# Performance work log

Hardware: AMD Instinct MI355X
Metric: run time of the kernel (lower is better)

Reference implementation:

```python
import jax, jax.numpy as jnp
import numpy as np
import math

H = 16          # num_head
HID = 1024      # hidden_size
D = HID // H    # per-head dim used in 1/sqrt(D) scaling


def _linear(x, w, b):
    # torch nn.Linear: y = x @ W^T + b, W: [out, in]
    return jnp.einsum('bld,od->blo', x, w) + b


def _split_heads(x):
    # [B, L, HID] -> [B*H, L, D] with index b*H + h (matches transpose_qkv)
    B, L, _ = x.shape
    return x.reshape(B, L, H, D).transpose(0, 2, 1, 3).reshape(B * H, L, D)


def _merge_heads(x, B):
    # [B*H, L, D] -> [B, L, HID] (matches restore_qkv)
    BH, L, d = x.shape
    return x.reshape(B, H, L, d).transpose(0, 2, 1, 3).reshape(B, L, H * d)


def setup_inputs() -> dict:
    key = jax.random.key(0)
    ks = jax.random.split(key, 16)
    B, L = 4, 1024
    inv = 1.0 / math.sqrt(HID)
    inp = {
        'queries': jax.random.normal(ks[0], (B, L, HID), jnp.float32),
        'keys':    jax.random.normal(ks[1], (B, L, HID), jnp.float32),
        'values':  jax.random.normal(ks[2], (B, L, HID), jnp.float32),
        'prev':    jax.random.normal(ks[3], (B * H, L, L), jnp.float32),
        'mask':    jax.random.randint(ks[4], (B, L), 1, L + 1, jnp.int64),
        'Wq_w': jax.random.uniform(ks[5], (HID, HID), jnp.float32, -inv, inv),
        'Wq_b': jax.random.uniform(ks[6], (HID,), jnp.float32, -inv, inv),
        'Wk_w': jax.random.uniform(ks[7], (HID, HID), jnp.float32, -inv, inv),
        'Wk_b': jax.random.uniform(ks[8], (HID,), jnp.float32, -inv, inv),
        'Wv_w': jax.random.uniform(ks[9], (HID, HID), jnp.float32, -inv, inv),
        'Wv_b': jax.random.uniform(ks[10], (HID,), jnp.float32, -inv, inv),
        'Wo_w': jax.random.uniform(ks[11], (HID, HID), jnp.float32, -inv, inv),
        'Wo_b': jax.random.uniform(ks[12], (HID,), jnp.float32, -inv, inv),
        'gat':  jnp.asarray(1.0, jnp.float32),
    }
    return inp


def reference(queries, keys, values, prev, mask,
              Wq_w, Wq_b, Wk_w, Wk_b, Wv_w, Wv_b, Wo_w, Wo_b, gat):
    B, L, _ = queries.shape
    q = _split_heads(_linear(queries, Wq_w, Wq_b))   # [BH, L, D]
    k = _split_heads(_linear(keys,    Wk_w, Wk_b))
    v = _split_heads(_linear(values,  Wv_w, Wv_b))

    scores = jnp.einsum('bqd,bkd->bqk', q, k)        # [BH, L, L]

    # residual score gate (learn_gat=True): scalar sigmoid blend
    g = jax.nn.sigmoid(gat)
    scores = prev * g + (1.0 - g) * scores

    # masking: torch repeats mask along dim0 (tile), arange(key_len) < lengths
    lens = jnp.tile(mask, (H, 1))                    # [BH, L]
    keep = jnp.arange(L)[None, None, :] < lens[:, :, None]  # [BH, L, L]
    masked = jnp.where(keep, scores, jnp.float32(-1e9)) / math.sqrt(D)
    probs = jax.nn.softmax(masked, axis=-1)          # dropout p=0 -> identity

    att = jnp.einsum('bqk,bkd->bqd', probs, v)       # [BH, L, D]
    out = _linear(_merge_heads(att, B), Wo_w, Wo_b)  # [B, L, HID]
    return out, scores
```

## Files before the change

kernel.cpp:

```cpp
#include <hip/hip_runtime.h>
#include <hip/hip_bf16.h>
#include <stdint.h>

#define AS1 __attribute__((address_space(1)))
#define AS3 __attribute__((address_space(3)))

typedef __bf16 bf16_t;
typedef bf16_t bf16x8 __attribute__((ext_vector_type(8)));
typedef float f32x4 __attribute__((ext_vector_type(4)));
typedef unsigned short u16;
typedef u16 u16x4 __attribute__((ext_vector_type(4)));

#define MFMA16(a, b, c) __builtin_amdgcn_mfma_f32_16x16x32_bf16(a, b, c, 0, 0, 0)

static __device__ __forceinline__ void gload_lds16(const void* g, void* l) {
    __builtin_amdgcn_global_load_lds((const AS1 void*)g, (AS3 void*)l, 16, 0, 0);
}

template <int ROW_SHIFT>
static __device__ __forceinline__ void stage16k(const char* g, char* lds, int gstride, int tid) {
    const int lane = tid & 63, w = tid >> 6;
#pragma unroll
    for (int i = 0; i < 4; ++i) {
        int chunk = w + i * 4;
        int p = chunk * 1024 + lane * 16;
        int row = p >> ROW_SHIFT;
        int col = (p & ((1 << ROW_SHIFT) - 1)) ^ ((row & 7) << 4);
        gload_lds16(g + row * gstride + col, lds + chunk * 1024);
    }
}

template <int ROW_SHIFT>
static __device__ __forceinline__ bf16x8 lds_frag(const char* lds, int row, int colb) {
    int off = (row << ROW_SHIFT) + (colb ^ ((row & 7) << 4));
    return *(const bf16x8*)(lds + off);
}

__global__ __launch_bounds__(256) void pack_bf16(
    const float* q, const float* k, const float* v,
    const float* wq, const float* wk, const float* wv, const float* wo,
    bf16_t* qb, bf16_t* kb, bf16_t* vb,
    bf16_t* wqb, bf16_t* wkb, bf16_t* wvb, bf16_t* wob) {
    const float* src; bf16_t* dst; int n;
    switch (blockIdx.y) {
        case 0: src = q;  dst = qb;  n = 4194304; break;
        case 1: src = k;  dst = kb;  n = 4194304; break;
        case 2: src = v;  dst = vb;  n = 4194304; break;
        case 3: src = wq; dst = wqb; n = 1048576; break;
        case 4: src = wk; dst = wkb; n = 1048576; break;
        case 5: src = wv; dst = wvb; n = 1048576; break;
        default: src = wo; dst = wob; n = 1048576; break;
    }
    int i = (blockIdx.x * 256 + threadIdx.x) * 8;
    if (i >= n) return;
    f32x4 v0 = *(const f32x4*)(src + i);
    f32x4 v1 = *(const f32x4*)(src + i + 4);
    bf16x8 o;
#pragma unroll
    for (int e = 0; e < 4; ++e) o[e] = (bf16_t)v0[e];
#pragma unroll
    for (int e = 0; e < 4; ++e) o[e + 4] = (bf16_t)v1[e];
    *(bf16x8*)(dst + i) = o;
}

template <int MODE>
__global__ __launch_bounds__(256, 2) void gemm_nt(
    const bf16_t* A0, const bf16_t* A1, const bf16_t* A2,
    const bf16_t* B0, const bf16_t* B1, const bf16_t* B2,
    const float* bias0, const float* bias1, const float* bias2,
    bf16_t* Qs, bf16_t* Ks, bf16_t* Vt, float* outF) {
    __shared__ __align__(1024) char sm[32768];
    const int tid = threadIdx.x, lane = tid & 63, w = tid >> 6;
    const int wr = w >> 1, wc = w & 1;
    const int m0 = blockIdx.y * 128, n0 = blockIdx.x * 128;
    const int z = (MODE == 0) ? blockIdx.z : 0;

    const bf16_t* A; const bf16_t* Bw; const float* bias;
    if (MODE == 0) {
        A    = (z == 0) ? A0 : (z == 1) ? A1 : A2;
        Bw   = (z == 0) ? B0 : (z == 1) ? B1 : B2;
        bias = (z == 0) ? bias0 : (z == 1) ? bias1 : bias2;
    } else { A = A0; Bw = B0; bias = bias0; }

    const char* Ab = (const char*)A + (size_t)m0 * 2048;
    const char* Bb = (const char*)Bw + (size_t)n0 * 2048;

    f32x4 acc[4][4] = {};
    for (int k0 = 0; k0 < 1024; k0 += 64) {
        stage16k<7>(Ab + k0 * 2, sm, 2048, tid);
        stage16k<7>(Bb + k0 * 2, sm + 16384, 2048, tid);
        __syncthreads();
#pragma unroll
        for (int kk = 0; kk < 2; ++kk) {
            bf16x8 af[4], bfr[4];
#pragma unroll
            for (int i = 0; i < 4; ++i)
                af[i] = lds_frag<7>(sm, wr * 64 + i * 16 + (lane & 15), kk * 64 + (lane >> 4) * 16);
#pragma unroll
            for (int j = 0; j < 4; ++j)
                bfr[j] = lds_frag<7>(sm + 16384, wc * 64 + j * 16 + (lane & 15), kk * 64 + (lane >> 4) * 16);
#pragma unroll
            for (int i = 0; i < 4; ++i)
#pragma unroll
                for (int j = 0; j < 4; ++j)
                    acc[i][j] = MFMA16(af[i], bfr[j], acc[i][j]);
        }
        __syncthreads();
    }

#pragma unroll
    for (int i = 0; i < 4; ++i) {
#pragma unroll
        for (int j = 0; j < 4; ++j) {
            const int mb = m0 + wr * 64 + i * 16 + ((lane >> 4) << 2);
            const int n = n0 + wc * 64 + j * 16 + (lane & 15);
            const float bv = bias[n];
            if (MODE == 1) {
#pragma unroll
                for (int r = 0; r < 4; ++r)
                    outF[(size_t)(mb + r) * 1024 + n] = acc[i][j][r] + bv;
            } else if (z == 2) {
                const int b = mb >> 10, l = mb & 1023;
                const int h = n >> 6, d = n & 63;
                u16x4 pk;
#pragma unroll
                for (int r = 0; r < 4; ++r) {
                    bf16_t x = (bf16_t)(acc[i][j][r] + bv);
                    pk[r] = __builtin_bit_cast(u16, x);
                }
                *(u16x4*)&Vt[((size_t)((b * 16 + h) * 64 + d)) * 1024 + l] = pk;
            } else {
                bf16_t* dst = (z == 0) ? Qs : Ks;
                const int h = n >> 6, d = n & 63;
#pragma unroll
                for (int r = 0; r < 4; ++r) {
                    const int m = mb + r, b = m >> 10, l = m & 1023;
                    dst[((size_t)((b * 16 + h) * 1024 + l)) * 64 + d] = (bf16_t)(acc[i][j][r] + bv);
                }
            }
        }
    }
}

__global__ __launch_bounds__(256) void attn_scores(
    const bf16_t* Qs, const bf16_t* Ks,
    const float* prev, const int* mask, const float* gatp,
    float* scoresOut, float* rowMax, float* rowSum) {
    const int tid = threadIdx.x, lane = tid & 63, w = tid >> 6;
    const int bh = blockIdx.y;
    const int q0 = blockIdx.x * 64 + w * 16;
    const float gv = gatp[0];
    const float g = 1.f / (1.f + __expf(-gv));
    const float og = 1.f - g;

    bf16x8 qa[2];
#pragma unroll
    for (int kk = 0; kk < 2; ++kk)
        qa[kk] = *(const bf16x8*)(Qs + ((size_t)(bh * 1024 + q0 + (lane & 15))) * 64 + kk * 32 + (lane >> 4) * 8);

    const int rq = q0 + ((lane >> 4) << 2);
    int len[4]; float mrun[4], lrun[4];
#pragma unroll
    for (int r = 0; r < 4; ++r) {
        len[r] = mask[(bh & 3) * 1024 + rq + r];
        mrun[r] = -1e30f;
        lrun[r] = 0.f;
    }

    const bf16_t* Kb = Ks + (size_t)bh * 65536;
    const float* prow = prev + ((size_t)(bh * 1024 + rq)) * 1024;
    float* srow = scoresOut + ((size_t)(bh * 1024 + rq)) * 1024;

    for (int kt = 0; kt < 8; ++kt) {
        const int kcb = kt * 128 + (lane & 15);
        float pf[8][4];
#pragma unroll
        for (int j = 0; j < 8; ++j)
#pragma unroll
            for (int r = 0; r < 4; ++r)
                pf[j][r] = prow[(size_t)r * 1024 + kcb + j * 16];

        f32x4 s[8] = {};
#pragma unroll
        for (int kk = 0; kk < 2; ++kk)
#pragma unroll
            for (int j = 0; j < 8; ++j) {
                bf16x8 bfr = *(const bf16x8*)(Kb + ((size_t)(kt * 128 + j * 16 + (lane & 15))) * 64 + kk * 32 + (lane >> 4) * 8);
                s[j] = MFMA16(qa[kk], bfr, s[j]);
            }

#pragma unroll
        for (int j = 0; j < 8; ++j)
#pragma unroll
            for (int r = 0; r < 4; ++r) {
                const float bl = g * pf[j][r] + og * s[j][r];
                srow[(size_t)r * 1024 + kcb + j * 16] = bl;
                s[j][r] = bl * 0.125f;
            }

#pragma unroll
        for (int r = 0; r < 4; ++r) {
            const int ln = len[r];
            float vm = -1e30f;
#pragma unroll
            for (int j = 0; j < 8; ++j)
                vm = fmaxf(vm, (kcb + j * 16 < ln) ? s[j][r] : -1e30f);
            vm = fmaxf(vm, __shfl_xor(vm, 1));
            vm = fmaxf(vm, __shfl_xor(vm, 2));
            vm = fmaxf(vm, __shfl_xor(vm, 4));
            vm = fmaxf(vm, __shfl_xor(vm, 8));
            const float mnew = fmaxf(mrun[r], vm);
            float es = 0.f;
#pragma unroll
            for (int j = 0; j < 8; ++j)
                es += (kcb + j * 16 < ln) ? __expf(s[j][r] - mnew) : 0.f;
            es += __shfl_xor(es, 1);
            es += __shfl_xor(es, 2);
            es += __shfl_xor(es, 4);
            es += __shfl_xor(es, 8);
            lrun[r] = lrun[r] * __expf(mrun[r] - mnew) + es;
            mrun[r] = mnew;
        }
    }
    if ((lane & 15) == 0) {
#pragma unroll
        for (int r = 0; r < 4; ++r) {
            rowMax[bh * 1024 + rq + r] = mrun[r];
            rowSum[bh * 1024 + rq + r] = lrun[r];
        }
    }
}

__global__ __launch_bounds__(256) void attn_pv(
    const float* scoresOut, const bf16_t* Vt,
    const int* mask, const float* rowMax, const float* rowSum,
    bf16_t* att) {
    const int tid = threadIdx.x, lane = tid & 63, w = tid >> 6;
    const int bh = blockIdx.y;
    const int q0 = blockIdx.x * 64 + w * 16;
    const int qrow = q0 + (lane & 15);
    const float mq = rowMax[bh * 1024 + qrow];
    const float il = 1.f / rowSum[bh * 1024 + qrow];
    const int len = mask[(bh & 3) * 1024 + qrow];

    const float* srow = scoresOut + ((size_t)(bh * 1024 + qrow)) * 1024;
    const bf16_t* Vb = Vt + (size_t)bh * 65536;

    f32x4 acc[4] = {};
    for (int kt = 0; kt < 8; ++kt) {
        const int kb0 = kt * 128 + (lane >> 4) * 8;
        f32x4 sv[4][2];
#pragma unroll
        for (int kk = 0; kk < 4; ++kk) {
            sv[kk][0] = *(const f32x4*)(srow + kb0 + kk * 32);
            sv[kk][1] = *(const f32x4*)(srow + kb0 + kk * 32 + 4);
        }
#pragma unroll
        for (int kk = 0; kk < 4; ++kk) {
            bf16x8 pa;
#pragma unroll
            for (int e = 0; e < 8; ++e) {
                const float vv = (e < 4) ? sv[kk][0][e] : sv[kk][1][e - 4];
                pa[e] = (bf16_t)((kb0 + kk * 32 + e < len) ? __expf(vv * 0.125f - mq) * il : 0.f);
            }
#pragma unroll
            for (int ni = 0; ni < 4; ++ni) {
                bf16x8 vb = *(const bf16x8*)(Vb + ((size_t)(ni * 16 + (lane & 15))) * 1024 + kt * 128 + kk * 32 + (lane >> 4) * 8);
                acc[ni] = MFMA16(pa, vb, acc[ni]);
            }
        }
    }
    const int b = bh >> 4, h = bh & 15;
    const int rq = q0 + ((lane >> 4) << 2);
#pragma unroll
    for (int ni = 0; ni < 4; ++ni) {
        const int d = ni * 16 + (lane & 15);
#pragma unroll
        for (int r = 0; r < 4; ++r)
            att[((size_t)(b * 1024 + rq + r)) * 1024 + h * 64 + d] = (bf16_t)acc[ni][r];
    }
}

extern "C" void kernel_launch(void* const* d_in, const int* in_sizes, int n_in,
                              void* d_out, int out_size, void* d_ws, size_t ws_size,
                              hipStream_t stream) {
    (void)in_sizes; (void)n_in; (void)out_size; (void)ws_size;
    const float* q    = (const float*)d_in[0];
    const float* k    = (const float*)d_in[1];
    const float* v    = (const float*)d_in[2];
    const float* prev = (const float*)d_in[3];
    const int*   mask = (const int*)d_in[4];
    const float* Wq_w = (const float*)d_in[5];
    const float* Wq_b = (const float*)d_in[6];
    const float* Wk_w = (const float*)d_in[7];
    const float* Wk_b = (const float*)d_in[8];
    const float* Wv_w = (const float*)d_in[9];
    const float* Wv_b = (const float*)d_in[10];
    const float* Wo_w = (const float*)d_in[11];
    const float* Wo_b = (const float*)d_in[12];
    const float* gat  = (const float*)d_in[13];

    float* outp   = (float*)d_out;
    float* scores = outp + 4194304;

    char* ws = (char*)d_ws;
    bf16_t* qb  = (bf16_t*)(ws + 0);
    bf16_t* kb  = (bf16_t*)(ws + 8388608);
    bf16_t* vb  = (bf16_t*)(ws + 16777216);
    bf16_t* wqb = (bf16_t*)(ws + 25165824);
    bf16_t* wkb = (bf16_t*)(ws + 27262976);
    bf16_t* wvb = (bf16_t*)(ws + 29360128);
    bf16_t* wob = (bf16_t*)(ws + 31457280);
    bf16_t* Qs  = (bf16_t*)(ws + 33554432);
    bf16_t* Ks  = (bf16_t*)(ws + 41943040);
    bf16_t* Vt  = (bf16_t*)(ws + 50331648);
    bf16_t* att = (bf16_t*)(ws + 58720256);
    float* rowMax = (float*)(ws + 67108864);
    float* rowSum = (float*)(ws + 67371008);

    pack_bf16<<<dim3(2048, 7), 256, 0, stream>>>(q, k, v, Wq_w, Wk_w, Wv_w, Wo_w,
                                                 qb, kb, vb, wqb, wkb, wvb, wob);
    gemm_nt<0><<<dim3(8, 32, 3), 256, 0, stream>>>(qb, kb, vb, wqb, wkb, wvb,
                                                   Wq_b, Wk_b, Wv_b, Qs, Ks, Vt, nullptr);
    attn_scores<<<dim3(16, 64), 256, 0, stream>>>(Qs, Ks, prev, mask, gat,
                                                  scores, rowMax, rowSum);
    attn_pv<<<dim3(16, 64), 256, 0, stream>>>(scores, Vt, mask, rowMax, rowSum, att);
    gemm_nt<1><<<dim3(8, 32, 1), 256, 0, stream>>>(att, nullptr, nullptr, wob, nullptr, nullptr,
                                                   Wo_b, nullptr, nullptr,
                                                   nullptr, nullptr, nullptr, outp);
}
```

Measured before the change: 745.0 us.

## Fuse score and PV kernels into single flash-style online-softmax attention kernel

After: 682.8 us. -8.3%, faster.

```diff
diff --git a/kernel.cpp b/kernel.cpp
--- a/kernel.cpp
+++ b/kernel.cpp
@@ -7,6 +7,7 @@
 
 typedef __bf16 bf16_t;
 typedef bf16_t bf16x8 __attribute__((ext_vector_type(8)));
+typedef bf16_t bf16x4 __attribute__((ext_vector_type(4)));
 typedef float f32x4 __attribute__((ext_vector_type(4)));
 typedef unsigned short u16;
 typedef u16 u16x4 __attribute__((ext_vector_type(4)));
@@ -142,143 +143,129 @@
     }
 }
 
-__global__ __launch_bounds__(256) void attn_scores(
-    const bf16_t* Qs, const bf16_t* Ks,
+__global__ __launch_bounds__(256) void attn_fused(
+    const bf16_t* Qs, const bf16_t* Ks, const bf16_t* Vt,
     const float* prev, const int* mask, const float* gatp,
-    float* scoresOut, float* rowMax, float* rowSum) {
+    float* scoresOut, bf16_t* att) {
+    __shared__ __align__(1024) char psm[16384];
     const int tid = threadIdx.x, lane = tid & 63, w = tid >> 6;
+    char* myP = psm + w * 4096;
     const int bh = blockIdx.y;
     const int q0 = blockIdx.x * 64 + w * 16;
-    const float gv = gatp[0];
-    const float g = 1.f / (1.f + __expf(-gv));
-    const float og = 1.f - g;
+    const int qc = lane & 15;
+    const int gq = lane >> 4;
+    const float gate = 1.f / (1.f + __expf(-gatp[0]));
+    const float og = 1.f - gate;
 
     bf16x8 qa[2];
 #pragma unroll
     for (int kk = 0; kk < 2; ++kk)
-        qa[kk] = *(const bf16x8*)(Qs + ((size_t)(bh * 1024 + q0 + (lane & 15))) * 64 + kk * 32 + (lane >> 4) * 8);
-
-    const int rq = q0 + ((lane >> 4) << 2);
-    int len[4]; float mrun[4], lrun[4];
-#pragma unroll
-    for (int r = 0; r < 4; ++r) {
-        len[r] = mask[(bh & 3) * 1024 + rq + r];
-        mrun[r] = -1e30f;
-        lrun[r] = 0.f;
-    }
+        qa[kk] = *(const bf16x8*)(Qs + ((size_t)(bh * 1024 + q0 + qc)) * 64 + kk * 32 + gq * 8);
+
+    const int len = mask[(bh & 3) * 1024 + q0 + qc];
+    float mrun = -1e30f, lrun = 0.f;
+    f32x4 acc[4] = {};
 
     const bf16_t* Kb = Ks + (size_t)bh * 65536;
-    const float* prow = prev + ((size_t)(bh * 1024 + rq)) * 1024;
-    float* srow = scoresOut + ((size_t)(bh * 1024 + rq)) * 1024;
+    const bf16_t* Vb = Vt + (size_t)bh * 65536;
+    const float* prow = prev + ((size_t)(bh * 1024 + q0 + qc)) * 1024;
+    float* srow = scoresOut + ((size_t)(bh * 1024 + q0 + qc)) * 1024;
 
     for (int kt = 0; kt < 8; ++kt) {
-        const int kcb = kt * 128 + (lane & 15);
-        float pf[8][4];
+        const int kb = kt * 128;
+        f32x4 pf[8];
 #pragma unroll
         for (int j = 0; j < 8; ++j)
+            pf[j] = *(const f32x4*)(prow + kb + j * 16 + gq * 4);
+
+        f32x4 s[8] = {};
+#pragma unroll
+        for (int kk = 0; kk < 2; ++kk)
+#pragma unroll
+            for (int j = 0; j < 8; ++j) {
+                bf16x8 ka = *(const bf16x8*)(Kb + ((size_t)(kb + j * 16 + qc)) * 64 + kk * 32 + gq * 8);
+                s[j] = MFMA16(ka, qa[kk], s[j]);
+            }
+
+#pragma unroll
+        for (int j = 0; j < 8; ++j) {
+            f32x4 bl;
+#pragma unroll
+            for (int r = 0; r < 4; ++r) bl[r] = gate * pf[j][r] + og * s[j][r];
+            *(f32x4*)(srow + kb + j * 16 + gq * 4) = bl;
 #pragma unroll
             for (int r = 0; r < 4; ++r)
-                pf[j][r] = prow[(size_t)r * 1024 + kcb + j * 16];
-
-        f32x4 s[8] = {};
-#pragma unroll
-        for (int kk = 0; kk < 2; ++kk)
-#pragma unroll
-            for (int j = 0; j < 8; ++j) {
-                bf16x8 bfr = *(const bf16x8*)(Kb + ((size_t)(kt * 128 + j * 16 + (lane & 15))) * 64 + kk * 32 + (lane >> 4) * 8);
-                s[j] = MFMA16(qa[kk], bfr, s[j]);
+                s[j][r] = (kb + j * 16 + gq * 4 + r < len) ? bl[r] * 0.125f : -1e30f;
+        }
+
+        float vm = -1e30f;
+#pragma unroll
+        for (int j = 0; j < 8; ++j)
+#pragma unroll
+            for (int r = 0; r < 4; ++r) vm = fmaxf(vm, s[j][r]);
+        vm = fmaxf(vm, __shfl_xor(vm, 16));
+        vm = fmaxf(vm, __shfl_xor(vm, 32));
+        const float mnew = fmaxf(mrun, vm);
+
+        float ps = 0.f;
+#pragma unroll
+        for (int j = 0; j < 8; ++j)
+#pragma unroll
+            for (int r = 0; r < 4; ++r) {
+                const float p = __expf(s[j][r] - mnew);
+                s[j][r] = p;
+                ps += p;
             }
-
-#pragma unroll
-        for (int j = 0; j < 8; ++j)
-#pragma unroll
-            for (int r = 0; r < 4; ++r) {
-                const float bl = g * pf[j][r] + og * s[j][r];
-                srow[(size_t)r * 1024 + kcb + j * 16] = bl;
-                s[j][r] = bl * 0.125f;
-            }
-
-#pragma unroll
-        for (int r = 0; r < 4; ++r) {
-            const int ln = len[r];
-            float vm = -1e30f;
-#pragma unroll
-            for (int j = 0; j < 8; ++j)
-                vm = fmaxf(vm, (kcb + j * 16 < ln) ? s[j][r] : -1e30f);
-            vm = fmaxf(vm, __shfl_xor(vm, 1));
-            vm = fmaxf(vm, __shfl_xor(vm, 2));
-            vm = fmaxf(vm, __shfl_xor(vm, 4));
-            vm = fmaxf(vm, __shfl_xor(vm, 8));
-            const float mnew = fmaxf(mrun[r], vm);
-            float es = 0.f;
-#pragma unroll
-            for (int j = 0; j < 8; ++j)
-                es += (kcb + j * 16 < ln) ? __expf(s[j][r] - mnew) : 0.f;
-            es += __shfl_xor(es, 1);
-            es += __shfl_xor(es, 2);
-            es += __shfl_xor(es, 4);
-            es += __shfl_xor(es, 8);
-            lrun[r] = lrun[r] * __expf(mrun[r] - mnew) + es;
-            mrun[r] = mnew;
-        }
-    }
-    if ((lane & 15) == 0) {
-#pragma unroll
-        for (int r = 0; r < 4; ++r) {
-            rowMax[bh * 1024 + rq + r] = mrun[r];
-            rowSum[bh * 1024 + rq + r] = lrun[r];
-        }
-    }
-}
-
-__global__ __launch_bounds__(256) void attn_pv(
-    const float* scoresOut, const bf16_t* Vt,
-    const int* mask, const float* rowMax, const float* rowSum,
-    bf16_t* att) {
-    const int tid = threadIdx.x, lane = tid & 63, w = tid >> 6;
-    const int bh = blockIdx.y;
-    const int q0 = blockIdx.x * 64 + w * 16;
-    const int qrow = q0 + (lane & 15);
-    const float mq = rowMax[bh * 1024 + qrow];
-    const float il = 1.f / rowSum[bh * 1024 + qrow];
-    const int len = mask[(bh & 3) * 1024 + qrow];
-
-    const float* srow = scoresOut + ((size_t)(bh * 1024 + qrow)) * 1024;
-    const bf16_t* Vb = Vt + (size_t)bh * 65536;
-
-    f32x4 acc[4] = {};
-    for (int kt = 0; kt < 8; ++kt) {
-        const int kb0 = kt * 128 + (lane >> 4) * 8;
-        f32x4 sv[4][2];
+        ps += __shfl_xor(ps, 16);
+        ps += __shfl_xor(ps, 32);
+        const float corr = __expf(mrun - mnew);
+        lrun = lrun * corr + ps;
+        mrun = mnew;
+
+        float cr[4];
+#pragma unroll
+        for (int r = 0; r < 4; ++r) cr[r] = __shfl(corr, gq * 4 + r);
+#pragma unroll
+        for (int ni = 0; ni < 4; ++ni)
+#pragma unroll
+            for (int r = 0; r < 4; ++r) acc[ni][r] *= cr[r];
+
+#pragma unroll
+        for (int j = 0; j < 8; ++j) {
+            bf16x4 pk;
+#pragma unroll
+            for (int r = 0; r < 4; ++r) pk[r] = (bf16_t)s[j][r];
+            int boff = qc * 256 + j * 32 + gq * 8;
+            boff ^= (qc & 7) << 4;
+            *(bf16x4*)(myP + boff) = pk;
+        }
+        asm volatile("s_waitcnt lgkmcnt(0)" ::: "memory");
+
 #pragma unroll
         for (int kk = 0; kk < 4; ++kk) {
-            sv[kk][0] = *(const f32x4*)(srow + kb0 + kk * 32);
-            sv[kk][1] = *(const f32x4*)(srow + kb0 + kk * 32 + 4);
-        }
-#pragma unroll
-        for (int kk = 0; kk < 4; ++kk) {
-            bf16x8 pa;
-#pragma unroll
-            for (int e = 0; e < 8; ++e) {
-                const float vv = (e < 4) ? sv[kk][0][e] : sv[kk][1][e - 4];
-                pa[e] = (bf16_t)((kb0 + kk * 32 + e < len) ? __expf(vv * 0.125f - mq) * il : 0.f);
-            }
+            int roff = qc * 256 + kk * 64 + gq * 16;
+            roff ^= (qc & 7) << 4;
+            const bf16x8 pa = *(const bf16x8*)(myP + roff);
 #pragma unroll
             for (int ni = 0; ni < 4; ++ni) {
-                bf16x8 vb = *(const bf16x8*)(Vb + ((size_t)(ni * 16 + (lane & 15))) * 1024 + kt * 128 + kk * 32 + (lane >> 4) * 8);
+                bf16x8 vb = *(const bf16x8*)(Vb + ((size_t)(ni * 16 + qc)) * 1024 + kb + kk * 32 + gq * 8);
                 acc[ni] = MFMA16(pa, vb, acc[ni]);
             }
         }
-    }
+        asm volatile("" ::: "memory");
+    }
+
+    const float il = 1.f / lrun;
+    float ir[4];
+#pragma unroll
+    for (int r = 0; r < 4; ++r) ir[r] = __shfl(il, gq * 4 + r);
     const int b = bh >> 4, h = bh & 15;
-    const int rq = q0 + ((lane >> 4) << 2);
-#pragma unroll
-    for (int ni = 0; ni < 4; ++ni) {
-        const int d = ni * 16 + (lane & 15);
+#pragma unroll
+    for (int ni = 0; ni < 4; ++ni)
 #pragma unroll
         for (int r = 0; r < 4; ++r)
-            att[((size_t)(b * 1024 + rq + r)) * 1024 + h * 64 + d] = (bf16_t)acc[ni][r];
-    }
+            att[((size_t)(b * 1024 + q0 + gq * 4 + r)) * 1024 + h * 64 + ni * 16 + qc] =
+                (bf16_t)(acc[ni][r] * ir[r]);
 }
 
 extern "C" void kernel_launch(void* const* d_in, const int* in_sizes, int n_in,
@@ -315,16 +302,13 @@
     bf16_t* Ks  = (bf16_t*)(ws + 41943040);
     bf16_t* Vt  = (bf16_t*)(ws + 50331648);
     bf16_t* att = (bf16_t*)(ws + 58720256);
-    float* rowMax = (float*)(ws + 67108864);
-    float* rowSum = (float*)(ws + 67371008);
 
     pack_bf16<<<dim3(2048, 7), 256, 0, stream>>>(q, k, v, Wq_w, Wk_w, Wv_w, Wo_w,
                                                  qb, kb, vb, wqb, wkb, wvb, wob);
     gemm_nt<0><<<dim3(8, 32, 3), 256, 0, stream>>>(qb, kb, vb, wqb, wkb, wvb,
                                                    Wq_b, Wk_b, Wv_b, Qs, Ks, Vt, nullptr);
-    attn_scores<<<dim3(16, 64), 256, 0, stream>>>(Qs, Ks, prev, mask, gat,
-                                                  scores, rowMax, rowSum);
-    attn_pv<<<dim3(16, 64), 256, 0, stream>>>(scores, Vt, mask, rowMax, rowSum, att);
+    attn_fused<<<dim3(16, 64), 256, 0, stream>>>(Qs, Ks, Vt, prev, mask, gat,
+                                                 scores, att);
     gemm_nt<1><<<dim3(8, 32, 1), 256, 0, stream>>>(att, nullptr, nullptr, wob, nullptr, nullptr,
                                                    Wo_b, nullptr, nullptr,
                                                    nullptr, nullptr, nullptr, outp);
```
